# Kernel tuning notes

Measured on AMD Instinct MI355X. Metric: run time of the kernel, lower is better.

## Reference

```python
import jax, jax.numpy as jnp
import numpy as np

N_NODES = 100000
N_EDGES = 1600000
N_GRAPHS = 512
IN_DIM = 128
D = 128
N_CLASSES = 10


def gcn_layer(x, src, dst, W, b, n_nodes):
    """PyG GCNConv: out = D^{-1/2}(A+I)D^{-1/2} (x W) + b, deg over dst col + self-loop."""
    h = x @ W  # [N, d]
    deg = jax.ops.segment_sum(jnp.ones(src.shape[0], x.dtype), dst,
                              num_segments=n_nodes) + 1.0  # self-loop adds 1
    dinv = jax.lax.rsqrt(deg)  # deg >= 1 so always finite
    norm = dinv[src] * dinv[dst]  # [E]
    agg = jax.ops.segment_sum(h[src] * norm[:, None], dst, num_segments=n_nodes)
    agg = agg + h * (dinv * dinv)[:, None]  # self-loop message: dinv_i^2 * h_i
    return agg + b


def setup_inputs() -> dict:
    key = jax.random.key(0)
    ks = jax.random.split(key, 10)
    s = 0.05
    return {
        "x": jax.random.normal(ks[0], (N_NODES, IN_DIM), jnp.float32),
        "c_2": jax.random.randint(ks[1], (N_EDGES,), 0, N_NODES, jnp.int64),
        "u_2": jax.random.randint(ks[2], (N_EDGES,), 0, N_NODES, jnp.int64),
        "batch": jnp.sort(jax.random.randint(ks[3], (N_NODES,), 0, N_GRAPHS, jnp.int64)),
        "W_enc": jax.random.normal(ks[4], (IN_DIM, D), jnp.float32) * s,
        "b_enc": jnp.zeros((D,), jnp.float32),
        "W1": jax.random.normal(ks[5], (D, D), jnp.float32) * s,
        "b1": jnp.zeros((D,), jnp.float32),
        "W2": jax.random.normal(ks[6], (D, D), jnp.float32) * s,
        "b2": jnp.zeros((D,), jnp.float32),
        "W3": jax.random.normal(ks[7], (D, D), jnp.float32) * s,
        "b3": jnp.zeros((D,), jnp.float32),
        "Wr1": jax.random.normal(ks[8], (D, D), jnp.float32) * s,
        "br1": jnp.zeros((D,), jnp.float32),
        "Wr2": jax.random.normal(ks[9], (D, N_CLASSES), jnp.float32) * s,
        "br2": jnp.zeros((N_CLASSES,), jnp.float32),
    }


def reference(x, c_2, u_2, batch, W_enc, b_enc, W1, b1, W2, b2, W3, b3,
              Wr1, br1, Wr2, br2):
    h = x @ W_enc + b_enc
    for W, b in ((W1, b1), (W2, b2), (W3, b3)):
        h = gcn_layer(h, c_2, u_2, W, b, N_NODES)
        h = jax.nn.relu(h)  # dropout is identity in eval mode
    # global_add_pool over graph assignment
    g = jax.ops.segment_sum(h, batch, num_segments=N_GRAPHS)  # [G, d]
    logits = jax.nn.relu(g @ Wr1 + br1) @ Wr2 + br2  # [G, num_classes]
    return logits
```

## Files before the change

kernel.cpp:

```cpp
#include <hip/hip_runtime.h>
#include <hip/hip_bf16.h>

#define NN 100000
#define NE 1600000
#define NG 512
#define NC 10
#define NBINS 196
#define BINCAP 10240
#define EPB 4096

typedef __attribute__((ext_vector_type(8))) short bf16x8;
typedef __attribute__((ext_vector_type(4))) float f32x4;
typedef int int4a __attribute__((ext_vector_type(4), aligned(4)));

__device__ __forceinline__ float bflo(unsigned u) { return __uint_as_float(u << 16); }
__device__ __forceinline__ float bfhi(unsigned u) { return __uint_as_float(u & 0xffff0000u); }
__device__ __forceinline__ unsigned short f2bf(float f) {
  unsigned u = __float_as_uint(f);
  unsigned r = u + 0x7fffu + ((u >> 16) & 1u);
  return (unsigned short)(r >> 16);
}


__global__ __launch_bounds__(256) void k_bininit(int* __restrict__ binCursor) {
  int t = blockIdx.x * 256 + threadIdx.x;
  if (t < NBINS) binCursor[t] = t * BINCAP;
}

__global__ __launch_bounds__(256) void k_binp1(const int* __restrict__ src, const int* __restrict__ dst,
                                               int* __restrict__ binCursor, uint2* __restrict__ stage) {
  __shared__ uint2 sstage[EPB];
  __shared__ int cnt[NBINS];
  __shared__ int pre[NBINS];
  __shared__ int base[NBINS];
  __shared__ int lcur[NBINS];
  int t = threadIdx.x;
  for (int i = t; i < NBINS; i += 256) { cnt[i] = 0; lcur[i] = 0; }
  __syncthreads();
  int e0 = blockIdx.x * EPB;
  int mybin[16];
  uint2 mypair[16];
#pragma unroll
  for (int i = 0; i < 16; ++i) {
    int e = e0 + i * 256 + t;
    if (e < NE) {
      int s = src[e], d = dst[e];
      mybin[i] = d >> 9;
      mypair[i] = make_uint2((unsigned)s, (unsigned)d);
      atomicAdd(&cnt[mybin[i]], 1);
    } else {
      mybin[i] = -1;
    }
  }
  __syncthreads();
  if (t == 0) {
    int run = 0;
    for (int b = 0; b < NBINS; ++b) { pre[b] = run; run += cnt[b]; }
  }
  __syncthreads();
  if (t < NBINS && cnt[t] > 0) base[t] = atomicAdd(&binCursor[t], cnt[t]);
  __syncthreads();
#pragma unroll
  for (int i = 0; i < 16; ++i) {
    if (mybin[i] >= 0) {
      int r = atomicAdd(&lcur[mybin[i]], 1);
      sstage[pre[mybin[i]] + r] = mypair[i];
    }
  }
  __syncthreads();
  int total = NE - e0; if (total > EPB) total = EPB;
  for (int sidx = t; sidx < total; sidx += 256) {
    uint2 pr = sstage[sidx];
    int b = (int)(pr.y >> 9);
    stage[base[b] + (sidx - pre[b])] = pr;
  }
}

__global__ __launch_bounds__(256) void k_binp2(const uint2* __restrict__ stage, const int* __restrict__ binCursor,
                                               int* __restrict__ csr_src, int* __restrict__ offs,
                                               int* __restrict__ deg, float* __restrict__ dinv) {
  __shared__ int ldeg[512];
  __shared__ int loff[512];
  __shared__ int part[256];
  int b = blockIdx.x;
  int t = threadIdx.x;
  int n0 = b << 9;
  int sbase = b * BINCAP;
  int cnt = binCursor[b] - sbase;
  for (int i = t; i < 512; i += 256) ldeg[i] = 0;
  __syncthreads();
  for (int j = t; j < cnt; j += 256) {
    int d = (int)stage[sbase + j].y;
    atomicAdd(&ldeg[d - n0], 1);
  }
  __syncthreads();
  int i2 = t * 2;
  int a0 = ldeg[i2], a1 = ldeg[i2 + 1];
  int s = a0 + a1;
  part[t] = s;
  __syncthreads();
  for (int o = 1; o < 256; o <<= 1) {
    int v = (t >= o) ? part[t - o] : 0;
    __syncthreads();
    part[t] += v;
    __syncthreads();
  }
  int ex = part[t] - s;
  loff[i2] = ex;
  loff[i2 + 1] = ex + a0;
  int nd0 = n0 + i2, nd1 = n0 + i2 + 1;
  if (nd0 < NN) { offs[nd0] = sbase + ex;      deg[nd0] = a0; dinv[nd0] = rsqrtf((float)a0 + 1.0f); }
  if (nd1 < NN) { offs[nd1] = sbase + ex + a0; deg[nd1] = a1; dinv[nd1] = rsqrtf((float)a1 + 1.0f); }
  ldeg[i2] = 0; ldeg[i2 + 1] = 0;
  __syncthreads();
  for (int j = t; j < cnt; j += 256) {
    uint2 p = stage[sbase + j];
    int li = (int)p.y - n0;
    int r = atomicAdd(&ldeg[li], 1);
    csr_src[sbase + loff[li] + r] = (int)p.x;
  }
}

__global__ __launch_bounds__(256) void k_wt4(const float* __restrict__ Wa, const float* __restrict__ Wb,
                                             const float* __restrict__ Wc, const float* __restrict__ Wd,
                                             unsigned short* __restrict__ Ta, unsigned short* __restrict__ Tb,
                                             unsigned short* __restrict__ Tc, unsigned short* __restrict__ Td) {
  int w = blockIdx.x >> 6;
  const float* W = (w == 0) ? Wa : (w == 1) ? Wb : (w == 2) ? Wc : Wd;
  unsigned short* T = (w == 0) ? Ta : (w == 1) ? Tb : (w == 2) ? Tc : Td;
  int idx = (blockIdx.x & 63) * 256 + threadIdx.x;
  int k = idx >> 7, c = idx & 127;
  T[c * 128 + k] = f2bf(W[k * 128 + c]);
}


template<int ADD_BIAS, int RELU, int SRC_F32, int SCALE_ROW>
__global__ __launch_bounds__(256) void k_gemm_mfma(const void* __restrict__ Ap,
                                                   const unsigned short* __restrict__ Wt,
                                                   const float* __restrict__ bias,
                                                   const float* __restrict__ dinv,
                                                   unsigned short* __restrict__ Out, int M) {
  __shared__ uint4 Al4[2048];
  __shared__ uint4 Wl4[2048];
  int row0 = blockIdx.x * 128;
  const uint4* W16 = (const uint4*)Wt;
#pragma unroll
  for (int it = 0; it < 8; ++it) {
    int idx = it * 256 + threadIdx.x;
    int r = idx >> 4, c = idx & 15;
    int gr = row0 + r;
    uint4 v = make_uint4(0, 0, 0, 0);
    if (gr < M) {
      if (SRC_F32) {
        const float4* Af = (const float4*)Ap;
        float4 f0 = Af[(size_t)gr * 32 + c * 2];
        float4 f1 = Af[(size_t)gr * 32 + c * 2 + 1];
        v.x = (unsigned)f2bf(f0.x) | ((unsigned)f2bf(f0.y) << 16);
        v.y = (unsigned)f2bf(f0.z) | ((unsigned)f2bf(f0.w) << 16);
        v.z = (unsigned)f2bf(f1.x) | ((unsigned)f2bf(f1.y) << 16);
        v.w = (unsigned)f2bf(f1.z) | ((unsigned)f2bf(f1.w) << 16);
      } else {
        v = ((const uint4*)Ap)[(size_t)gr * 16 + c];
      }
    }
    Al4[r * 16 + (c ^ (r & 15))] = v;
    Wl4[r * 16 + (c ^ (r & 15))] = W16[idx];
  }
  __syncthreads();

  int lane = threadIdx.x & 63;
  int wid = threadIdx.x >> 6;
  int wr = wid >> 1, wc = wid & 1;
  int lr = lane & 15, kb = lane >> 4;

  f32x4 acc[4][4] = {};
#pragma unroll
  for (int ks = 0; ks < 4; ++ks) {
    int c = ks * 4 + kb;
    bf16x8 af[4], bfr[4];
#pragma unroll
    for (int i = 0; i < 4; ++i) {
      int ar = wr * 64 + i * 16 + lr;
      af[i] = *(const bf16x8*)&Al4[ar * 16 + (c ^ lr)];
      int bc = wc * 64 + i * 16 + lr;
      bfr[i] = *(const bf16x8*)&Wl4[bc * 16 + (c ^ lr)];
    }
#pragma unroll
    for (int i = 0; i < 4; ++i)
#pragma unroll
      for (int n = 0; n < 4; ++n)
        acc[i][n] = __builtin_amdgcn_mfma_f32_16x16x32_bf16(af[i], bfr[n], acc[i][n], 0, 0, 0);
  }

  float bcol[4];
  if (ADD_BIAS) {
#pragma unroll
    for (int n = 0; n < 4; ++n) bcol[n] = bias[wc * 64 + n * 16 + lr];
  }
#pragma unroll
  for (int i = 0; i < 4; ++i) {
    int rbase = row0 + wr * 64 + i * 16 + kb * 4;
#pragma unroll
    for (int n = 0; n < 4; ++n) {
      int col = wc * 64 + n * 16 + lr;
#pragma unroll
      for (int j = 0; j < 4; ++j) {
        int gr = rbase + j;
        if (gr < M) {
          float v = acc[i][n][j];
          if (ADD_BIAS) v += bcol[n];
          if (RELU) v = fmaxf(v, 0.f);
          if (SCALE_ROW) v *= dinv[gr];
          Out[(size_t)gr * 128 + col] = f2bf(v);
        }
      }
    }
  }
}


__global__ __launch_bounds__(256) void k_agg(const unsigned short* __restrict__ hs,
                                             const int* __restrict__ offs, const int* __restrict__ deg,
                                             const float* __restrict__ dinv,
                                             const int* __restrict__ csr_src,
                                             const float* __restrict__ bias,
                                             unsigned short* __restrict__ out) {
  int node = blockIdx.x * 4 + (threadIdx.x >> 6);
  if (node >= NN) return;
  int l = threadIdx.x & 63;
  const unsigned* hs32 = (const unsigned*)hs;
  float di = dinv[node];
  unsigned v = hs32[(size_t)node * 64 + l];
  float ax = bflo(v), ay = bfhi(v);
  int p0 = offs[node], n = deg[node];
  int p = 0;
  for (; p + 16 <= n; p += 16) {
    const int* cp = csr_src + p0 + p;
    int4a i0 = *(const int4a*)cp;
    int4a i1 = *(const int4a*)(cp + 4);
    int4a i2 = *(const int4a*)(cp + 8);
    int4a i3 = *(const int4a*)(cp + 12);
    unsigned u0  = hs32[(size_t)i0.x * 64 + l], u1  = hs32[(size_t)i0.y * 64 + l];
    unsigned u2  = hs32[(size_t)i0.z * 64 + l], u3  = hs32[(size_t)i0.w * 64 + l];
    unsigned u4  = hs32[(size_t)i1.x * 64 + l], u5  = hs32[(size_t)i1.y * 64 + l];
    unsigned u6  = hs32[(size_t)i1.z * 64 + l], u7  = hs32[(size_t)i1.w * 64 + l];
    unsigned u8  = hs32[(size_t)i2.x * 64 + l], u9  = hs32[(size_t)i2.y * 64 + l];
    unsigned u10 = hs32[(size_t)i2.z * 64 + l], u11 = hs32[(size_t)i2.w * 64 + l];
    unsigned u12 = hs32[(size_t)i3.x * 64 + l], u13 = hs32[(size_t)i3.y * 64 + l];
    unsigned u14 = hs32[(size_t)i3.z * 64 + l], u15 = hs32[(size_t)i3.w * 64 + l];
    ax += bflo(u0) + bflo(u1) + bflo(u2) + bflo(u3) + bflo(u4) + bflo(u5) + bflo(u6) + bflo(u7)
        + bflo(u8) + bflo(u9) + bflo(u10) + bflo(u11) + bflo(u12) + bflo(u13) + bflo(u14) + bflo(u15);
    ay += bfhi(u0) + bfhi(u1) + bfhi(u2) + bfhi(u3) + bfhi(u4) + bfhi(u5) + bfhi(u6) + bfhi(u7)
        + bfhi(u8) + bfhi(u9) + bfhi(u10) + bfhi(u11) + bfhi(u12) + bfhi(u13) + bfhi(u14) + bfhi(u15);
  }
  for (; p + 8 <= n; p += 8) {
    const int* cp = csr_src + p0 + p;
    int4a i0 = *(const int4a*)cp;
    int4a i1 = *(const int4a*)(cp + 4);
    unsigned u0 = hs32[(size_t)i0.x * 64 + l], u1 = hs32[(size_t)i0.y * 64 + l];
    unsigned u2 = hs32[(size_t)i0.z * 64 + l], u3 = hs32[(size_t)i0.w * 64 + l];
    unsigned u4 = hs32[(size_t)i1.x * 64 + l], u5 = hs32[(size_t)i1.y * 64 + l];
    unsigned u6 = hs32[(size_t)i1.z * 64 + l], u7 = hs32[(size_t)i1.w * 64 + l];
    ax += bflo(u0) + bflo(u1) + bflo(u2) + bflo(u3) + bflo(u4) + bflo(u5) + bflo(u6) + bflo(u7);
    ay += bfhi(u0) + bfhi(u1) + bfhi(u2) + bfhi(u3) + bfhi(u4) + bfhi(u5) + bfhi(u6) + bfhi(u7);
  }
  for (; p < n; ++p) {
    int s0 = csr_src[p0 + p];
    unsigned u0 = hs32[(size_t)s0 * 64 + l];
    ax += bflo(u0);
    ay += bfhi(u0);
  }
  float2 b2 = ((const float2*)bias)[l];
  ax = fmaxf(fmaf(ax, di, b2.x), 0.f);
  ay = fmaxf(fmaf(ay, di, b2.y), 0.f);
  ((unsigned*)out)[(size_t)node * 64 + l] = (unsigned)f2bf(ax) | ((unsigned)f2bf(ay) << 16);
}


__device__ __forceinline__ int lowerb(const int* a, int n, int key) {
  int lo = 0, hi = n;
  while (lo < hi) {
    int mid = (lo + hi) >> 1;
    if (a[mid] < key) lo = mid + 1; else hi = mid;
  }
  return lo;
}

__global__ __launch_bounds__(256) void k_pool(const unsigned short* __restrict__ h, const int* __restrict__ batch,
                                              float* __restrict__ g) {
  __shared__ float sx[4][64];
  __shared__ float sy[4][64];
  int gi = blockIdx.x;
  int col = threadIdx.x & 63;
  int rp = threadIdx.x >> 6;
  int lo = lowerb(batch, NN, gi), hi = lowerb(batch, NN, gi + 1);
  const unsigned* h32 = (const unsigned*)h;
  float ax = 0.f, ay = 0.f;
  for (int i = lo + rp; i < hi; i += 4) {
    unsigned u = h32[(size_t)i * 64 + col];
    ax += bflo(u);
    ay += bfhi(u);
  }
  sx[rp][col] = ax;
  sy[rp][col] = ay;
  __syncthreads();
  if (rp == 0) {
    ax = sx[0][col] + sx[1][col] + sx[2][col] + sx[3][col];
    ay = sy[0][col] + sy[1][col] + sy[2][col] + sy[3][col];
    ((float2*)g)[gi * 64 + col] = make_float2(ax, ay);
  }
}

__global__ __launch_bounds__(256) void k_gemm_f32(const float* __restrict__ A, const float* __restrict__ W,
                                                  const float* __restrict__ bias, float* __restrict__ Out,
                                                  int M) {
  __shared__ float4 Wl[128 * 32];
  __shared__ float4 Xl[128 * 32];
  const float4* W4 = (const float4*)W;
  for (int i = threadIdx.x; i < 4096; i += 256) Wl[i] = W4[i];
  int row0 = blockIdx.x * 128;
  const float4* A4 = (const float4*)A;
  for (int i = threadIdx.x; i < 4096; i += 256) {
    int r = i >> 5, g = i & 31;
    int gr = row0 + r;
    float4 v = make_float4(0.f, 0.f, 0.f, 0.f);
    if (gr < M) v = A4[gr * 32 + g];
    Xl[r * 32 + (g ^ ((r >> 3) & 7))] = v;
  }
  __syncthreads();

  int cg = threadIdx.x & 15;
  int rg = threadIdx.x >> 4;
  int swz = rg & 7;
  float acc[8][8] = {};
  for (int g = 0; g < 32; ++g) {
    float4 xv[8];
#pragma unroll
    for (int i = 0; i < 8; ++i) xv[i] = Xl[(rg * 8 + i) * 32 + (g ^ swz)];
#pragma unroll
    for (int kk = 0; kk < 4; ++kk) {
      float4 wa = Wl[(g * 4 + kk) * 32 + cg * 2];
      float4 wb = Wl[(g * 4 + kk) * 32 + cg * 2 + 1];
#pragma unroll
      for (int i = 0; i < 8; ++i) {
        float x = (kk == 0) ? xv[i].x : (kk == 1) ? xv[i].y : (kk == 2) ? xv[i].z : xv[i].w;
        acc[i][0] = fmaf(x, wa.x, acc[i][0]);
        acc[i][1] = fmaf(x, wa.y, acc[i][1]);
        acc[i][2] = fmaf(x, wa.z, acc[i][2]);
        acc[i][3] = fmaf(x, wa.w, acc[i][3]);
        acc[i][4] = fmaf(x, wb.x, acc[i][4]);
        acc[i][5] = fmaf(x, wb.y, acc[i][5]);
        acc[i][6] = fmaf(x, wb.z, acc[i][6]);
        acc[i][7] = fmaf(x, wb.w, acc[i][7]);
      }
    }
  }
  float4 ba = ((const float4*)bias)[cg * 2];
  float4 bb = ((const float4*)bias)[cg * 2 + 1];
#pragma unroll
  for (int i = 0; i < 8; ++i) {
    int gr = row0 + rg * 8 + i;
    if (gr < M) {
      float4 oa, ob;
      oa.x = fmaxf(acc[i][0] + ba.x, 0.f); oa.y = fmaxf(acc[i][1] + ba.y, 0.f);
      oa.z = fmaxf(acc[i][2] + ba.z, 0.f); oa.w = fmaxf(acc[i][3] + ba.w, 0.f);
      ob.x = fmaxf(acc[i][4] + bb.x, 0.f); ob.y = fmaxf(acc[i][5] + bb.y, 0.f);
      ob.z = fmaxf(acc[i][6] + bb.z, 0.f); ob.w = fmaxf(acc[i][7] + bb.w, 0.f);
      ((float4*)Out)[gr * 32 + cg * 2] = oa;
      ((float4*)Out)[gr * 32 + cg * 2 + 1] = ob;
    }
  }
}

__global__ __launch_bounds__(128) void k_cls(const float* __restrict__ t, const float* __restrict__ Wr2,
                                             const float* __restrict__ br2, float* __restrict__ out) {
  int gi = blockIdx.x;
  __shared__ float row[128];
  row[threadIdx.x] = t[gi * 128 + threadIdx.x];
  __syncthreads();
  if (threadIdx.x < NC) {
    float acc = br2[threadIdx.x];
    for (int k = 0; k < 128; ++k) acc = fmaf(row[k], Wr2[k * NC + threadIdx.x], acc);
    out[gi * NC + threadIdx.x] = acc;
  }
}


extern "C" void kernel_launch(void* const* d_in, const int* in_sizes, int n_in,
                              void* d_out, int out_size, void* d_ws, size_t ws_size,
                              hipStream_t stream) {
  const float* x     = (const float*)d_in[0];
  const int*   src   = (const int*)d_in[1];
  const int*   dst   = (const int*)d_in[2];
  const int*   batch = (const int*)d_in[3];
  const float* W_enc = (const float*)d_in[4];
  const float* b_enc = (const float*)d_in[5];
  const float* W1 = (const float*)d_in[6],  *b1 = (const float*)d_in[7];
  const float* W2 = (const float*)d_in[8],  *b2 = (const float*)d_in[9];
  const float* W3 = (const float*)d_in[10], *b3 = (const float*)d_in[11];
  const float* Wr1 = (const float*)d_in[12], *br1 = (const float*)d_in[13];
  const float* Wr2 = (const float*)d_in[14], *br2 = (const float*)d_in[15];
  float* out = (float*)d_out;

  char* ws = (char*)d_ws;
  size_t off = 0;
  auto alloc = [&](size_t bytes) {
    void* p = ws + off;
    off = (off + bytes + 255) & ~(size_t)255;
    return p;
  };
  unsigned short* h   = (unsigned short*)alloc((size_t)NN * 128 * 2);
  unsigned short* hs  = (unsigned short*)alloc((size_t)NN * 128 * 2);
  unsigned short* WtE = (unsigned short*)alloc(128 * 128 * 2);
  unsigned short* Wt1 = (unsigned short*)alloc(128 * 128 * 2);
  unsigned short* Wt2 = (unsigned short*)alloc(128 * 128 * 2);
  unsigned short* Wt3 = (unsigned short*)alloc(128 * 128 * 2);
  int*   deg      = (int*)alloc((size_t)NN * 4);
  float* dinv     = (float*)alloc((size_t)NN * 4);
  int*   offs     = (int*)alloc((size_t)NN * 4);
  int*   binCursor= (int*)alloc(NBINS * 4);
  int*   csr_src  = (int*)alloc((size_t)NBINS * BINCAP * 4);
  uint2* stage    = (uint2*)alloc((size_t)NBINS * BINCAP * 8);
  float* g        = (float*)alloc((size_t)NG * 128 * 4);
  float* t1       = (float*)alloc((size_t)NG * 128 * 4);

  k_bininit<<<1, 256, 0, stream>>>(binCursor);
  k_binp1<<<(NE + EPB - 1) / EPB, 256, 0, stream>>>(src, dst, binCursor, stage);
  k_binp2<<<NBINS, 256, 0, stream>>>(stage, binCursor, csr_src, offs, deg, dinv);

  k_wt4<<<256, 256, 0, stream>>>(W_enc, W1, W2, W3, WtE, Wt1, Wt2, Wt3);

  int gM = (NN + 127) / 128;
  k_gemm_mfma<1, 0, 1, 0><<<gM, 256, 0, stream>>>(x, WtE, b_enc, nullptr, h, NN);

  const unsigned short* Wts[3] = {Wt1, Wt2, Wt3};
  const float* bs[3] = {b1, b2, b3};
  int gA = (NN + 3) / 4;
  for (int L = 0; L < 3; ++L) {
    k_gemm_mfma<0, 0, 0, 1><<<gM, 256, 0, stream>>>(h, Wts[L], nullptr, dinv, hs, NN);
    k_agg<<<gA, 256, 0, stream>>>(hs, offs, deg, dinv, csr_src, bs[L], h);
  }

  k_pool<<<NG, 256, 0, stream>>>(h, batch, g);
  k_gemm_f32<<<(NG + 127) / 128, 256, 0, stream>>>(g, Wr1, br1, t1, NG);
  k_cls<<<NG, 128, 0, stream>>>(t1, Wr2, br2, out);
}
```

Before: 436.1 us.

## Pack edge records into 32 bits and sort bins by source in CSR build

Edge staging records are packed into one 32-bit word (source index shifted left by 9, plus the local destination offset), which halves stage traffic. Pass 1 now handles 8192 edges per block with a parallel prefix scan instead of a serial one. Pass 2 adds a counting sort of each bin's edges by source bucket in shared memory before the CSR scatter, so the neighbour lists come out roughly ordered by source. That ordering should improve gather locality in the later aggregation. The cost is extra shared memory (a 40KB sorted buffer) and more sync-heavy scans, and the code assumes source indices fit in 23 bits.

```diff
diff --git a/kernel.cpp b/kernel.cpp
--- a/kernel.cpp
+++ b/kernel.cpp
@@ -7,7 +7,7 @@
 #define NC 10
 #define NBINS 196
 #define BINCAP 10240
-#define EPB 4096
+#define EPB 8192
 
 typedef __attribute__((ext_vector_type(8))) short bf16x8;
 typedef __attribute__((ext_vector_type(4))) float f32x4;
@@ -23,101 +23,110 @@
 
 
 __global__ __launch_bounds__(256) void k_bininit(int* __restrict__ binCursor) {
-  int t = blockIdx.x * 256 + threadIdx.x;
+  int t = threadIdx.x;
   if (t < NBINS) binCursor[t] = t * BINCAP;
 }
 
 __global__ __launch_bounds__(256) void k_binp1(const int* __restrict__ src, const int* __restrict__ dst,
-                                               int* __restrict__ binCursor, uint2* __restrict__ stage) {
-  __shared__ uint2 sstage[EPB];
-  __shared__ int cnt[NBINS];
-  __shared__ int pre[NBINS];
-  __shared__ int base[NBINS];
-  __shared__ int lcur[NBINS];
+                                               int* __restrict__ binCursor, unsigned* __restrict__ stage) {
+  __shared__ unsigned srec[EPB];
+  __shared__ unsigned char sbin[EPB];
+  __shared__ int cnt[NBINS], pre[NBINS], base[NBINS], lcur[NBINS];
+  __shared__ int tmp[256];
   int t = threadIdx.x;
-  for (int i = t; i < NBINS; i += 256) { cnt[i] = 0; lcur[i] = 0; }
+  if (t < NBINS) { cnt[t] = 0; lcur[t] = 0; }
   __syncthreads();
   int e0 = blockIdx.x * EPB;
-  int mybin[16];
-  uint2 mypair[16];
-#pragma unroll
-  for (int i = 0; i < 16; ++i) {
+  unsigned myrec[32];
+  short mybin[32];
+#pragma unroll
+  for (int i = 0; i < 32; ++i) {
     int e = e0 + i * 256 + t;
     if (e < NE) {
       int s = src[e], d = dst[e];
-      mybin[i] = d >> 9;
-      mypair[i] = make_uint2((unsigned)s, (unsigned)d);
-      atomicAdd(&cnt[mybin[i]], 1);
-    } else {
-      mybin[i] = -1;
-    }
-  }
-  __syncthreads();
-  if (t == 0) {
-    int run = 0;
-    for (int b = 0; b < NBINS; ++b) { pre[b] = run; run += cnt[b]; }
-  }
-  __syncthreads();
-  if (t < NBINS && cnt[t] > 0) base[t] = atomicAdd(&binCursor[t], cnt[t]);
-  __syncthreads();
-#pragma unroll
-  for (int i = 0; i < 16; ++i) {
-    if (mybin[i] >= 0) {
-      int r = atomicAdd(&lcur[mybin[i]], 1);
-      sstage[pre[mybin[i]] + r] = mypair[i];
+      int b = d >> 9;
+      mybin[i] = (short)b;
+      myrec[i] = ((unsigned)s << 9) | (unsigned)(d & 511);
+      atomicAdd(&cnt[b], 1);
+    } else mybin[i] = -1;
+  }
+  __syncthreads();
+  int c0 = (t < NBINS) ? cnt[t] : 0;
+  tmp[t] = c0;
+  __syncthreads();
+  for (int o = 1; o < 256; o <<= 1) { int v = (t >= o) ? tmp[t - o] : 0; __syncthreads(); tmp[t] += v; __syncthreads(); }
+  if (t < NBINS) pre[t] = tmp[t] - c0;
+  __syncthreads();
+  if (t < NBINS && c0 > 0) base[t] = atomicAdd(&binCursor[t], c0);
+  __syncthreads();
+#pragma unroll
+  for (int i = 0; i < 32; ++i) {
+    int b = mybin[i];
+    if (b >= 0) {
+      int r = atomicAdd(&lcur[b], 1);
+      int pos = pre[b] + r;
+      srec[pos] = myrec[i];
+      sbin[pos] = (unsigned char)b;
     }
   }
   __syncthreads();
   int total = NE - e0; if (total > EPB) total = EPB;
   for (int sidx = t; sidx < total; sidx += 256) {
-    uint2 pr = sstage[sidx];
-    int b = (int)(pr.y >> 9);
-    stage[base[b] + (sidx - pre[b])] = pr;
-  }
-}
-
-__global__ __launch_bounds__(256) void k_binp2(const uint2* __restrict__ stage, const int* __restrict__ binCursor,
+    int b = sbin[sidx];
+    stage[base[b] + (sidx - pre[b])] = srec[sidx];
+  }
+}
+
+__global__ __launch_bounds__(256) void k_binp2(const unsigned* __restrict__ stage, const int* __restrict__ binCursor,
                                                int* __restrict__ csr_src, int* __restrict__ offs,
                                                int* __restrict__ deg, float* __restrict__ dinv) {
-  __shared__ int ldeg[512];
-  __shared__ int loff[512];
-  __shared__ int part[256];
-  int b = blockIdx.x;
-  int t = threadIdx.x;
+  __shared__ int ldeg[512], loff[512], lcur[512];
+  __shared__ int sbc[NBINS], sbb[NBINS];
+  __shared__ int tmp[256];
+  __shared__ unsigned sorted[BINCAP];
+  int b = blockIdx.x, t = threadIdx.x;
   int n0 = b << 9;
   int sbase = b * BINCAP;
-  int cnt = binCursor[b] - sbase;
-  for (int i = t; i < 512; i += 256) ldeg[i] = 0;
+  int cnt = binCursor[b] - sbase; if (cnt > BINCAP) cnt = BINCAP;
+  for (int i = t; i < 512; i += 256) { ldeg[i] = 0; lcur[i] = 0; }
+  if (t < NBINS) sbc[t] = 0;
   __syncthreads();
   for (int j = t; j < cnt; j += 256) {
-    int d = (int)stage[sbase + j].y;
-    atomicAdd(&ldeg[d - n0], 1);
+    unsigned r = stage[sbase + j];
+    atomicAdd(&ldeg[r & 511], 1);
+    atomicAdd(&sbc[r >> 18], 1);
   }
   __syncthreads();
   int i2 = t * 2;
   int a0 = ldeg[i2], a1 = ldeg[i2 + 1];
   int s = a0 + a1;
-  part[t] = s;
-  __syncthreads();
-  for (int o = 1; o < 256; o <<= 1) {
-    int v = (t >= o) ? part[t - o] : 0;
-    __syncthreads();
-    part[t] += v;
-    __syncthreads();
-  }
-  int ex = part[t] - s;
+  tmp[t] = s;
+  __syncthreads();
+  for (int o = 1; o < 256; o <<= 1) { int v = (t >= o) ? tmp[t - o] : 0; __syncthreads(); tmp[t] += v; __syncthreads(); }
+  int ex = tmp[t] - s;
   loff[i2] = ex;
   loff[i2 + 1] = ex + a0;
   int nd0 = n0 + i2, nd1 = n0 + i2 + 1;
   if (nd0 < NN) { offs[nd0] = sbase + ex;      deg[nd0] = a0; dinv[nd0] = rsqrtf((float)a0 + 1.0f); }
   if (nd1 < NN) { offs[nd1] = sbase + ex + a0; deg[nd1] = a1; dinv[nd1] = rsqrtf((float)a1 + 1.0f); }
-  ldeg[i2] = 0; ldeg[i2 + 1] = 0;
+  __syncthreads();
+  int c0 = (t < NBINS) ? sbc[t] : 0;
+  tmp[t] = c0;
+  __syncthreads();
+  for (int o = 1; o < 256; o <<= 1) { int v = (t >= o) ? tmp[t - o] : 0; __syncthreads(); tmp[t] += v; __syncthreads(); }
+  if (t < NBINS) { sbb[t] = tmp[t] - c0; sbc[t] = 0; }
   __syncthreads();
   for (int j = t; j < cnt; j += 256) {
-    uint2 p = stage[sbase + j];
-    int li = (int)p.y - n0;
-    int r = atomicAdd(&ldeg[li], 1);
-    csr_src[sbase + loff[li] + r] = (int)p.x;
+    unsigned r = stage[sbase + j];
+    int bk = r >> 18;
+    sorted[sbb[bk] + atomicAdd(&sbc[bk], 1)] = r;
+  }
+  __syncthreads();
+  for (int j = t; j < cnt; j += 256) {
+    unsigned r = sorted[j];
+    int li = r & 511;
+    int pos = atomicAdd(&lcur[li], 1);
+    csr_src[sbase + loff[li] + pos] = (int)(r >> 9);
   }
 }
 
@@ -420,7 +429,7 @@
   int*   offs     = (int*)alloc((size_t)NN * 4);
   int*   binCursor= (int*)alloc(NBINS * 4);
   int*   csr_src  = (int*)alloc((size_t)NBINS * BINCAP * 4);
-  uint2* stage    = (uint2*)alloc((size_t)NBINS * BINCAP * 8);
+  unsigned* stage = (unsigned*)alloc((size_t)NBINS * BINCAP * 4);
   float* g        = (float*)alloc((size_t)NG * 128 * 4);
   float* t1       = (float*)alloc((size_t)NG * 128 * 4);
 
```

New measurement: 437.9 us. Within noise of the previous version (+0.4%).
